# Optimization experiments

Hardware: AMD Instinct MI355X
Metric: run time of the kernel (lower is better)

## Reference

```python
import jax, jax.numpy as jnp
import numpy as np
import math

CH = 16      # scalar channels (Rs = [(16, 0)])
HEADS = 2
NB = 10      # number_of_basis for key/conv radial nets
HD = 100     # hidden width h
NBV = 3      # value radial basis (hard-coded in AttentionConvolution)
HDV = 100    # value radial hidden width
MAXR = 5.0
EPS = 1e-12  # safe-norm epsilon (r_eps analogue)


def swish(x):
    return x * jax.nn.sigmoid(x)


def cosine_basis(d, nb, max_radius):
    # CosineBasisModel basis: cos(pi/2 * (d - r_i)/step) on |.| < 1, else 0
    radii = jnp.linspace(0.0, max_radius, nb)
    step = radii[1] - radii[0]
    diff = (d[..., None] - radii) / step
    return jnp.where(jnp.abs(diff) < 1.0, jnp.cos(0.5 * math.pi * diff), 0.0)


def radial2(d, W0, W1, Wf, nb):
    # 2-hidden-layer radial MLP (L=2), swish activations, linear readout
    b = cosine_basis(d, nb, MAXR)
    hdn = swish(b @ W0)
    hdn = swish(hdn @ W1)
    return hdn @ Wf


def radial1(d, W0, Wf, nb):
    # 1-hidden-layer radial MLP (value branch, L=1)
    b = cosine_basis(d, nb, MAXR)
    return swish(b @ W0) @ Wf


def setup_inputs() -> dict:
    key = jax.random.key(0)
    ks = jax.random.split(key, 11)
    z, N = 2, 256

    def gn(k, shape, fan_in):
        return jax.random.normal(k, shape, jnp.float32) * (fan_in ** -0.5)

    return {
        "features": jax.random.normal(ks[0], (z, N, CH), jnp.float32),
        "xyz": jax.random.uniform(ks[1], (z, N, 3), jnp.float32) * MAXR,
        "Wq": gn(ks[2], (HEADS, CH, CH), CH),
        "K0": gn(ks[3], (HEADS, NB, HD), NB),
        "K1": gn(ks[4], (HEADS, HD, HD), HD),
        "Kf": gn(ks[5], (HEADS, HD, CH * CH), HD),
        "V0": gn(ks[6], (HEADS, NBV, HDV), NBV),
        "Vf": gn(ks[7], (HEADS, HDV, CH * CH), HDV),
        "C0": gn(ks[8], (NB, HD), NB),
        "C1": gn(ks[9], (HD, HD), HD),
        "Cf": gn(ks[10], (HD, CH * CH), HD),
    }


def reference(features, xyz, Wq, K0, K1, Kf, V0, Vf, C0, C1, Cf):
    z, N, ch = features.shape
    # rb - ra : rel[z, a, b] = xyz[b] - xyz[a]
    rel = xyz[:, None, :, :] - xyz[:, :, None, :]          # [z, a, b, 3]
    d = jnp.sqrt(jnp.sum(rel * rel, axis=-1) + EPS)        # [z, a, b]

    out = jnp.zeros_like(features)
    for h in range(HEADS):  # structurally distinct heads (distinct params)
        k = radial2(d, K0[h], K1[h], Kf[h], NB).reshape(z, N, N, ch, ch)
        v = radial1(d, V0[h], Vf[h], NBV).reshape(z, N, N, ch, ch)
        key_t = jnp.einsum('zabij,zbj->zabi', k, features)
        val_t = jnp.einsum('zabij,zbj->zabi', v, features)
        q = jnp.einsum('zai,oi->zao', features, Wq[h])     # Linear(Rs, Rs)
        scores = jnp.einsum('zabi,zai->zab', key_t, q) / ch
        p = jax.nn.softmax(scores, axis=-1)
        out = out + jnp.einsum('zab,zabi->zai', p, val_t)

    # final equivariant convolution: kernel(d) contracted over neighbors b
    kc = radial2(d, C0, C1, Cf, NB).reshape(z, N, N, ch, ch)
    return jnp.einsum('zabij,zbj->zai', kc, out)
```

## Files before the change

### kernel.cpp

```cpp
#include <hip/hip_runtime.h>
#include <hip/hip_fp16.h>
#include <math.h>

#define Z 2
#define NPT 256
#define CHN 16
#define NH 2
#define NBK 10
#define HD 100
#define NBV 3
#define G 512
#define VD 7.5f

__device__ __forceinline__ float swishf(float x) {
    return x / (1.0f + __expf(-x));
}

__device__ __forceinline__ float dot8(uint4 u, float4 a, float4 b) {
    float2 c0 = __half22float2(*(const __half2*)&u.x);
    float2 c1 = __half22float2(*(const __half2*)&u.y);
    float2 c2 = __half22float2(*(const __half2*)&u.z);
    float2 c3 = __half22float2(*(const __half2*)&u.w);
    return c0.x*a.x + c0.y*a.y + c1.x*a.z + c1.y*a.w
         + c2.x*b.x + c2.y*b.y + c3.x*b.z + c3.y*b.w;
}

__global__ __launch_bounds__(128)
void build_tables(const float* __restrict__ K0, const float* __restrict__ K1,
                  const float* __restrict__ C0, const float* __restrict__ C1,
                  const float* __restrict__ V0,
                  float* __restrict__ TKf, float* __restrict__ TCf,
                  float* __restrict__ TVf, float* __restrict__ out_zero) {
    int bid = blockIdx.x;
    int rep = bid >> 5;
    int g0  = (bid & 31) * 16;
    int t   = threadIdx.x;

    if (bid == 0) {
        float4* o4 = (float4*)out_zero;
        #pragma unroll
        for (int k = 0; k < 16; ++k) o4[k*128 + t] = make_float4(0.f,0.f,0.f,0.f);
    }

    if (rep >= 3) {
        const float* W0v = V0 + (rep - 3)*NBV*HD;
        float* Tf = TVf + (size_t)(rep - 3)*2*G*HD;
        if (t < HD) {
            #pragma unroll
            for (int k = 0; k < 16; ++k) {
                int gg = g0 + k;
                float d = gg * (VD / (float)(G-1));
                float s = 0.f;
                #pragma unroll
                for (int q = 0; q < NBV; ++q) {
                    float diff = (d - q*2.5f) * 0.4f;
                    float bq = (fabsf(diff) < 1.0f) ? __cosf(1.57079632679f*diff) : 0.f;
                    s += bq * W0v[q*HD + t];
                }
                float v = swishf(s);
                Tf[2*((size_t)gg*HD + t) + 0] = v;
                if (gg > 0) Tf[2*((size_t)(gg-1)*HD + t) + 1] = v;
            }
        }
        return;
    }

    const float* W0 = (rep == 0) ? K0 : (rep == 1) ? (K0 + NBK*HD) : C0;
    const float* W1 = (rep == 0) ? K1 : (rep == 1) ? (K1 + HD*HD)  : C1;
    float* Tf       = (rep == 0) ? TKf : (rep == 1) ? (TKf + 2*(size_t)G*HD) : TCf;

    __shared__ float s_b10[16][NBK];
    __shared__ __align__(16) float s_h1[HD*16];

    if (t < 16) {
        float d = (g0 + t) * (VD / (float)(G-1));
        #pragma unroll
        for (int q = 0; q < NBK; ++q) {
            float diff = (d - q*(5.0f/9.0f)) * 1.8f;
            s_b10[t][q] = (fabsf(diff) < 1.0f) ? __cosf(1.57079632679f*diff) : 0.f;
        }
    }
    __syncthreads();
    if (t < HD) {
        int n = t;
        float w[NBK];
        #pragma unroll
        for (int q = 0; q < NBK; ++q) w[q] = W0[q*HD + n];
        #pragma unroll
        for (int k = 0; k < 16; ++k) {
            float s = 0.f;
            #pragma unroll
            for (int q = 0; q < NBK; ++q) s += s_b10[k][q] * w[q];
            s_h1[n*16 + k] = swishf(s);
        }
    }
    __syncthreads();
    if (t < HD) {
        int m = t;
        float acc[16];
        #pragma unroll
        for (int k = 0; k < 16; ++k) acc[k] = 0.f;
        const float* w1 = W1 + m;
        #pragma unroll 2
        for (int n = 0; n < HD; ++n) {
            float w = w1[n*HD];
            const float4* hp = (const float4*)&s_h1[n*16];
            float4 x0 = hp[0], x1 = hp[1], x2 = hp[2], x3 = hp[3];
            acc[0]+=x0.x*w;  acc[1]+=x0.y*w;  acc[2]+=x0.z*w;  acc[3]+=x0.w*w;
            acc[4]+=x1.x*w;  acc[5]+=x1.y*w;  acc[6]+=x1.z*w;  acc[7]+=x1.w*w;
            acc[8]+=x2.x*w;  acc[9]+=x2.y*w;  acc[10]+=x2.z*w; acc[11]+=x2.w*w;
            acc[12]+=x3.x*w; acc[13]+=x3.y*w; acc[14]+=x3.z*w; acc[15]+=x3.w*w;
        }
        #pragma unroll
        for (int k = 0; k < 16; ++k) {
            float v = swishf(acc[k]);
            int gg = g0 + k;
            Tf[2*((size_t)gg*HD + m) + 0] = v;
            if (gg > 0) Tf[2*((size_t)(gg-1)*HD + m) + 1] = v;
        }
    }
}

__global__ __launch_bounds__(256)
void build_mats(const float* __restrict__ TK, const float* __restrict__ TC,
                const float* __restrict__ TV,
                const float* __restrict__ Kf, const float* __restrict__ Cf,
                const float* __restrict__ Vf,
                __half* __restrict__ MK, __half* __restrict__ MV,
                __half* __restrict__ MC) {
    int bid = blockIdx.x;
    int rep = bid >> 7;
    int g0  = (bid & 127) * 4;
    int t   = threadIdx.x;

    const float *T, *Wf;
    __half* M;
    if (rep == 0)      { T=TK;                    Wf=Kf;          M=MK; }
    else if (rep == 1) { T=TK+2*(size_t)G*HD;     Wf=Kf+HD*256;   M=MK+(size_t)G*256; }
    else if (rep == 2) { T=TC;                    Wf=Cf;          M=MC; }
    else if (rep == 3) { T=TV;                    Wf=Vf;          M=MV; }
    else               { T=TV+2*(size_t)G*HD;     Wf=Vf+HD*256;   M=MV+(size_t)G*256; }

    __shared__ float s_h[4][HD];
    for (int idx = t; idx < 4*HD; idx += 256) {
        int gp = idx / HD, m = idx - gp*HD;
        s_h[gp][m] = T[2*((size_t)(g0+gp)*HD + m)];
    }
    __syncthreads();

    float a0=0.f, a1=0.f, a2=0.f, a3=0.f;
    for (int m = 0; m < HD; ++m) {
        float w = Wf[m*256 + t];
        a0 += s_h[0][m]*w; a1 += s_h[1][m]*w;
        a2 += s_h[2][m]*w; a3 += s_h[3][m]*w;
    }
    int i = t >> 4, j = t & 15;
    int c = j >> 3, e = j & 7;
    size_t off = (size_t)(c*16 + i)*8 + e;
    M[(size_t)(g0+0)*256 + off] = __float2half(a0);
    M[(size_t)(g0+1)*256 + off] = __float2half(a1);
    M[(size_t)(g0+2)*256 + off] = __float2half(a2);
    M[(size_t)(g0+3)*256 + off] = __float2half(a3);
}

__global__ __launch_bounds__(256, 4)
void fused_attn(const float* __restrict__ f, const float* __restrict__ xyz,
                const float* __restrict__ Wq,
                const __half* __restrict__ MK, const __half* __restrict__ MV,
                float* __restrict__ attn_h) {
    int bid = blockIdx.x;
    int a  = bid & 255;
    int zh = bid >> 8;
    int h  = zh & 1;
    int z  = zh >> 1;
    int t  = threadIdx.x;

    __shared__ __align__(16) float s_f[NPT*CHN];
    __shared__ int   s_gi[NPT];
    __shared__ float s_fr[NPT];
    __shared__ float s_sc[NPT];
    __shared__ float s_q[16];
    __shared__ float s_red[8];
    __shared__ float s_red2[256];

    {
        const float4* fz = (const float4*)(f + (size_t)z*NPT*CHN);
        float4* sf = (float4*)s_f;
        for (int idx = t; idx < NPT*CHN/4; idx += 256) sf[idx] = fz[idx];
    }
    {
        float ax = xyz[(z*NPT + a)*3 + 0];
        float ay = xyz[(z*NPT + a)*3 + 1];
        float az = xyz[(z*NPT + a)*3 + 2];
        int b = t;
        float dx = xyz[(z*NPT + b)*3 + 0] - ax;
        float dy = xyz[(z*NPT + b)*3 + 1] - ay;
        float dz = xyz[(z*NPT + b)*3 + 2] - az;
        float d = sqrtf(dx*dx + dy*dy + dz*dz + 1e-12f);
        float fd = d * ((float)(G-1) / VD);
        int   gi = (int)fd;
        float fr = fd - (float)gi;
        if (gi >= G-1) { gi = G-2; fr = 1.0f; }
        s_gi[b] = gi; s_fr[b] = fr;
    }
    __syncthreads();
    if (t < CHN) {
        float s = 0.f;
        const float* wq = Wq + (h*CHN + t)*CHN;
        for (int i = 0; i < CHN; ++i) s += s_f[a*CHN + i] * wq[i];
        s_q[t] = s;
    }
    __syncthreads();

    int Gr = t >> 4;
    int i  = t & 15;
    float qi = s_q[i];
    int b0 = Gr*16;

    {
        const __half* basek = MK + (size_t)h*G*256;
        for (int k = 0; k < 16; ++k) {
            int b = b0 + k;
            const uint4* p = (const uint4*)(basek + (size_t)s_gi[b]*256) + i;
            uint4 q0 = p[0];
            uint4 q1 = p[16];
            uint4 q2 = p[32];
            uint4 q3 = p[48];
            float fr = s_fr[b];
            const float4* fp = (const float4*)&s_f[b*CHN];
            float4 f0=fp[0], f1=fp[1], f2=fp[2], f3=fp[3];
            float y0 = dot8(q0, f0, f1) + dot8(q1, f2, f3);
            float y1 = dot8(q2, f0, f1) + dot8(q3, f2, f3);
            float sc = qi * (y0 + fr*(y1 - y0));
            sc += __shfl_xor(sc, 1);
            sc += __shfl_xor(sc, 2);
            sc += __shfl_xor(sc, 4);
            sc += __shfl_xor(sc, 8);
            if (i == 0) s_sc[b] = sc * (1.0f/16.0f);
        }
    }
    __syncthreads();

    {
        float v = s_sc[t];
        float mx = v;
        for (int off = 32; off >= 1; off >>= 1) mx = fmaxf(mx, __shfl_xor(mx, off));
        int wid = t >> 6;
        if ((t & 63) == 0) s_red[wid] = mx;
        __syncthreads();
        mx = fmaxf(fmaxf(s_red[0], s_red[1]), fmaxf(s_red[2], s_red[3]));
        float e = __expf(v - mx);
        float s = e;
        for (int off = 32; off >= 1; off >>= 1) s += __shfl_xor(s, off);
        if ((t & 63) == 0) s_red[4 + wid] = s;
        __syncthreads();
        float tot = s_red[4] + s_red[5] + s_red[6] + s_red[7];
        s_sc[t] = e / tot;
    }
    __syncthreads();

    {
        const __half* basev = MV + (size_t)h*G*256;
        float o = 0.f;
        for (int k = 0; k < 16; ++k) {
            int b = b0 + k;
            const uint4* p = (const uint4*)(basev + (size_t)s_gi[b]*256) + i;
            uint4 q0 = p[0];
            uint4 q1 = p[16];
            uint4 q2 = p[32];
            uint4 q3 = p[48];
            float fr = s_fr[b];
            const float4* fp = (const float4*)&s_f[b*CHN];
            float4 f0=fp[0], f1=fp[1], f2=fp[2], f3=fp[3];
            float y0 = dot8(q0, f0, f1) + dot8(q1, f2, f3);
            float y1 = dot8(q2, f0, f1) + dot8(q3, f2, f3);
            o += s_sc[b] * (y0 + fr*(y1 - y0));
        }
        s_red2[Gr*16 + i] = o;
    }
    __syncthreads();
    if (t < 16) {
        float s = 0.f;
        for (int gp = 0; gp < 16; ++gp) s += s_red2[gp*16 + t];
        attn_h[(size_t)bid*CHN + t] = s;
    }
}

__global__ __launch_bounds__(256)
void conv_kernel(const float* __restrict__ xyz, const __half* __restrict__ MC,
                 const float* __restrict__ attn_h, float* __restrict__ out) {
    int bid = blockIdx.x;
    int bh  = bid & 1;
    int za  = bid >> 1;
    int z   = za >> 8;
    int b0g = bh * 128;
    int t   = threadIdx.x;

    __shared__ __align__(16) float s_ao[128*CHN];
    __shared__ int   s_gi[128];
    __shared__ float s_fr[128];
    __shared__ float s_red2[256];

    for (int idx = t; idx < 128*CHN; idx += 256) {
        s_ao[idx] = attn_h[(size_t)(z*NH + 0)*NPT*CHN + b0g*CHN + idx]
                  + attn_h[(size_t)(z*NH + 1)*NPT*CHN + b0g*CHN + idx];
    }
    if (t < 128) {
        int b = b0g + t;
        float dx = xyz[(z*NPT+b)*3+0] - xyz[za*3+0];
        float dy = xyz[(z*NPT+b)*3+1] - xyz[za*3+1];
        float dz = xyz[(z*NPT+b)*3+2] - xyz[za*3+2];
        float d = sqrtf(dx*dx + dy*dy + dz*dz + 1e-12f);
        float fd = d * ((float)(G-1) / VD);
        int   gi = (int)fd;
        float fr = fd - (float)gi;
        if (gi >= G-1) { gi = G-2; fr = 1.0f; }
        s_gi[t] = gi; s_fr[t] = fr;
    }
    __syncthreads();

    int Gr = t >> 4;
    int i  = t & 15;
    int l0 = Gr*8;
    {
        float o = 0.f;
        for (int k = 0; k < 8; ++k) {
            int l = l0 + k;
            const uint4* p = (const uint4*)(MC + (size_t)s_gi[l]*256) + i;
            uint4 q0 = p[0];
            uint4 q1 = p[16];
            uint4 q2 = p[32];
            uint4 q3 = p[48];
            float fr = s_fr[l];
            const float4* ap = (const float4*)&s_ao[l*CHN];
            float4 a0=ap[0], a1=ap[1], a2=ap[2], a3=ap[3];
            float y0 = dot8(q0, a0, a1) + dot8(q1, a2, a3);
            float y1 = dot8(q2, a0, a1) + dot8(q3, a2, a3);
            o += y0 + fr*(y1 - y0);
        }
        s_red2[Gr*16 + i] = o;
    }
    __syncthreads();
    if (t < 16) {
        float s = 0.f;
        for (int gp = 0; gp < 16; ++gp) s += s_red2[gp*16 + t];
        atomicAdd(out + (size_t)za*CHN + t, s);
    }
}

extern "C" void kernel_launch(void* const* d_in, const int* in_sizes, int n_in,
                              void* d_out, int out_size, void* d_ws, size_t ws_size,
                              hipStream_t stream) {
    const float* f   = (const float*)d_in[0];
    const float* xyz = (const float*)d_in[1];
    const float* Wq  = (const float*)d_in[2];
    const float* K0  = (const float*)d_in[3];
    const float* K1  = (const float*)d_in[4];
    const float* Kf  = (const float*)d_in[5];
    const float* V0  = (const float*)d_in[6];
    const float* Vf  = (const float*)d_in[7];
    const float* C0  = (const float*)d_in[8];
    const float* C1  = (const float*)d_in[9];
    const float* Cf  = (const float*)d_in[10];
    float* out = (float*)d_out;

    float2* TK2    = (float2*)d_ws;
    float2* TC2    = TK2 + (size_t)NH*G*HD;
    float2* TV2    = TC2 + (size_t)G*HD;
    __half* MK     = (__half*)(TV2 + (size_t)NH*G*HD);
    __half* MV     = MK + (size_t)NH*G*256;
    __half* MC     = MV + (size_t)NH*G*256;
    float*  attn_h = (float*)(MC + (size_t)G*256);

    build_tables<<<160,      128, 0, stream>>>(K0, K1, C0, C1, V0,
                                               (float*)TK2, (float*)TC2,
                                               (float*)TV2, out);
    build_mats  <<<640,      256, 0, stream>>>((const float*)TK2, (const float*)TC2,
                                               (const float*)TV2, Kf, Cf, Vf,
                                               MK, MV, MC);
    fused_attn  <<<Z*NH*NPT, 256, 0, stream>>>(f, xyz, Wq, MK, MV, attn_h);
    conv_kernel <<<Z*NPT*2,  256, 0, stream>>>(xyz, MC, attn_h, out);
}
```

Baseline: 132.7 us.

## Fuse radial table and matrix builds; interleave key/value matrices for single gather

Merges the two precompute kernels into one, so each block runs the radial MLP hidden layers and the final readout into half-precision matrices directly. This removes a launch and the intermediate float tables in global memory. Key and value matrices are now interleaved per grid point, so the attention kernel fetches both in one gather pass. It computes the value projections alongside the scores, keeps them in registers and reuses them after the softmax instead of gathering a second time. In exchange, the readout stage runs on 160 blocks of 128 threads instead of 640 blocks of 256, which lowers parallelism there. The extra 16 live values per thread also raise register pressure in the attention kernel.

```diff
diff --git a/kernel.cpp b/kernel.cpp
--- a/kernel.cpp
+++ b/kernel.cpp
@@ -26,11 +26,13 @@
 }
 
 __global__ __launch_bounds__(128)
-void build_tables(const float* __restrict__ K0, const float* __restrict__ K1,
-                  const float* __restrict__ C0, const float* __restrict__ C1,
-                  const float* __restrict__ V0,
-                  float* __restrict__ TKf, float* __restrict__ TCf,
-                  float* __restrict__ TVf, float* __restrict__ out_zero) {
+void build_all(const float* __restrict__ K0, const float* __restrict__ K1,
+               const float* __restrict__ Kf,
+               const float* __restrict__ C0, const float* __restrict__ C1,
+               const float* __restrict__ Cf,
+               const float* __restrict__ V0, const float* __restrict__ Vf,
+               __half* __restrict__ MKV, __half* __restrict__ MC,
+               float* __restrict__ out_zero) {
     int bid = blockIdx.x;
     int rep = bid >> 5;
     int g0  = (bid & 31) * 16;
@@ -42,9 +44,12 @@
         for (int k = 0; k < 16; ++k) o4[k*128 + t] = make_float4(0.f,0.f,0.f,0.f);
     }
 
+    __shared__ float s_b10[16][NBK];
+    __shared__ __align__(16) float s_h1[HD*16];
+    __shared__ float s_h2[16][HD];
+
     if (rep >= 3) {
         const float* W0v = V0 + (rep - 3)*NBV*HD;
-        float* Tf = TVf + (size_t)(rep - 3)*2*G*HD;
         if (t < HD) {
             #pragma unroll
             for (int k = 0; k < 16; ++k) {
@@ -57,116 +62,88 @@
                     float bq = (fabsf(diff) < 1.0f) ? __cosf(1.57079632679f*diff) : 0.f;
                     s += bq * W0v[q*HD + t];
                 }
-                float v = swishf(s);
-                Tf[2*((size_t)gg*HD + t) + 0] = v;
-                if (gg > 0) Tf[2*((size_t)(gg-1)*HD + t) + 1] = v;
+                s_h2[k][t] = swishf(s);
             }
         }
-        return;
-    }
-
-    const float* W0 = (rep == 0) ? K0 : (rep == 1) ? (K0 + NBK*HD) : C0;
-    const float* W1 = (rep == 0) ? K1 : (rep == 1) ? (K1 + HD*HD)  : C1;
-    float* Tf       = (rep == 0) ? TKf : (rep == 1) ? (TKf + 2*(size_t)G*HD) : TCf;
-
-    __shared__ float s_b10[16][NBK];
-    __shared__ __align__(16) float s_h1[HD*16];
-
-    if (t < 16) {
-        float d = (g0 + t) * (VD / (float)(G-1));
-        #pragma unroll
-        for (int q = 0; q < NBK; ++q) {
-            float diff = (d - q*(5.0f/9.0f)) * 1.8f;
-            s_b10[t][q] = (fabsf(diff) < 1.0f) ? __cosf(1.57079632679f*diff) : 0.f;
-        }
-    }
-    __syncthreads();
-    if (t < HD) {
-        int n = t;
-        float w[NBK];
-        #pragma unroll
-        for (int q = 0; q < NBK; ++q) w[q] = W0[q*HD + n];
-        #pragma unroll
-        for (int k = 0; k < 16; ++k) {
-            float s = 0.f;
-            #pragma unroll
-            for (int q = 0; q < NBK; ++q) s += s_b10[k][q] * w[q];
-            s_h1[n*16 + k] = swishf(s);
-        }
-    }
-    __syncthreads();
-    if (t < HD) {
-        int m = t;
-        float acc[16];
-        #pragma unroll
-        for (int k = 0; k < 16; ++k) acc[k] = 0.f;
-        const float* w1 = W1 + m;
-        #pragma unroll 2
-        for (int n = 0; n < HD; ++n) {
-            float w = w1[n*HD];
-            const float4* hp = (const float4*)&s_h1[n*16];
-            float4 x0 = hp[0], x1 = hp[1], x2 = hp[2], x3 = hp[3];
-            acc[0]+=x0.x*w;  acc[1]+=x0.y*w;  acc[2]+=x0.z*w;  acc[3]+=x0.w*w;
-            acc[4]+=x1.x*w;  acc[5]+=x1.y*w;  acc[6]+=x1.z*w;  acc[7]+=x1.w*w;
-            acc[8]+=x2.x*w;  acc[9]+=x2.y*w;  acc[10]+=x2.z*w; acc[11]+=x2.w*w;
-            acc[12]+=x3.x*w; acc[13]+=x3.y*w; acc[14]+=x3.z*w; acc[15]+=x3.w*w;
-        }
-        #pragma unroll
-        for (int k = 0; k < 16; ++k) {
-            float v = swishf(acc[k]);
-            int gg = g0 + k;
-            Tf[2*((size_t)gg*HD + m) + 0] = v;
-            if (gg > 0) Tf[2*((size_t)(gg-1)*HD + m) + 1] = v;
-        }
-    }
-}
-
-__global__ __launch_bounds__(256)
-void build_mats(const float* __restrict__ TK, const float* __restrict__ TC,
-                const float* __restrict__ TV,
-                const float* __restrict__ Kf, const float* __restrict__ Cf,
-                const float* __restrict__ Vf,
-                __half* __restrict__ MK, __half* __restrict__ MV,
-                __half* __restrict__ MC) {
-    int bid = blockIdx.x;
-    int rep = bid >> 7;
-    int g0  = (bid & 127) * 4;
-    int t   = threadIdx.x;
-
-    const float *T, *Wf;
-    __half* M;
-    if (rep == 0)      { T=TK;                    Wf=Kf;          M=MK; }
-    else if (rep == 1) { T=TK+2*(size_t)G*HD;     Wf=Kf+HD*256;   M=MK+(size_t)G*256; }
-    else if (rep == 2) { T=TC;                    Wf=Cf;          M=MC; }
-    else if (rep == 3) { T=TV;                    Wf=Vf;          M=MV; }
-    else               { T=TV+2*(size_t)G*HD;     Wf=Vf+HD*256;   M=MV+(size_t)G*256; }
-
-    __shared__ float s_h[4][HD];
-    for (int idx = t; idx < 4*HD; idx += 256) {
-        int gp = idx / HD, m = idx - gp*HD;
-        s_h[gp][m] = T[2*((size_t)(g0+gp)*HD + m)];
-    }
-    __syncthreads();
-
-    float a0=0.f, a1=0.f, a2=0.f, a3=0.f;
-    for (int m = 0; m < HD; ++m) {
-        float w = Wf[m*256 + t];
-        a0 += s_h[0][m]*w; a1 += s_h[1][m]*w;
-        a2 += s_h[2][m]*w; a3 += s_h[3][m]*w;
-    }
-    int i = t >> 4, j = t & 15;
-    int c = j >> 3, e = j & 7;
-    size_t off = (size_t)(c*16 + i)*8 + e;
-    M[(size_t)(g0+0)*256 + off] = __float2half(a0);
-    M[(size_t)(g0+1)*256 + off] = __float2half(a1);
-    M[(size_t)(g0+2)*256 + off] = __float2half(a2);
-    M[(size_t)(g0+3)*256 + off] = __float2half(a3);
+    } else {
+        const float* W0 = (rep == 0) ? K0 : (rep == 1) ? (K0 + NBK*HD) : C0;
+        const float* W1 = (rep == 0) ? K1 : (rep == 1) ? (K1 + HD*HD)  : C1;
+
+        if (t < 16) {
+            float d = (g0 + t) * (VD / (float)(G-1));
+            #pragma unroll
+            for (int q = 0; q < NBK; ++q) {
+                float diff = (d - q*(5.0f/9.0f)) * 1.8f;
+                s_b10[t][q] = (fabsf(diff) < 1.0f) ? __cosf(1.57079632679f*diff) : 0.f;
+            }
+        }
+        __syncthreads();
+        if (t < HD) {
+            int n = t;
+            float w[NBK];
+            #pragma unroll
+            for (int q = 0; q < NBK; ++q) w[q] = W0[q*HD + n];
+            #pragma unroll
+            for (int k = 0; k < 16; ++k) {
+                float s = 0.f;
+                #pragma unroll
+                for (int q = 0; q < NBK; ++q) s += s_b10[k][q] * w[q];
+                s_h1[n*16 + k] = swishf(s);
+            }
+        }
+        __syncthreads();
+        if (t < HD) {
+            int m = t;
+            float acc[16];
+            #pragma unroll
+            for (int k = 0; k < 16; ++k) acc[k] = 0.f;
+            const float* w1 = W1 + m;
+            #pragma unroll 2
+            for (int n = 0; n < HD; ++n) {
+                float w = w1[n*HD];
+                const float4* hp = (const float4*)&s_h1[n*16];
+                float4 x0 = hp[0], x1 = hp[1], x2 = hp[2], x3 = hp[3];
+                acc[0]+=x0.x*w;  acc[1]+=x0.y*w;  acc[2]+=x0.z*w;  acc[3]+=x0.w*w;
+                acc[4]+=x1.x*w;  acc[5]+=x1.y*w;  acc[6]+=x1.z*w;  acc[7]+=x1.w*w;
+                acc[8]+=x2.x*w;  acc[9]+=x2.y*w;  acc[10]+=x2.z*w; acc[11]+=x2.w*w;
+                acc[12]+=x3.x*w; acc[13]+=x3.y*w; acc[14]+=x3.z*w; acc[15]+=x3.w*w;
+            }
+            #pragma unroll
+            for (int k = 0; k < 16; ++k) s_h2[k][m] = swishf(acc[k]);
+        }
+    }
+    __syncthreads();
+
+    const float* Wf = (rep == 0) ? Kf
+                    : (rep == 1) ? (Kf + HD*256)
+                    : (rep == 2) ? Cf
+                    : (rep == 3) ? Vf : (Vf + HD*256);
+    __half* dst  = (rep == 2) ? MC  : (MKV + (size_t)((rep == 1 || rep == 4) ? 1 : 0)*G*512);
+    int    voff  = (rep >= 3) ? 256 : 0;
+    int    strd  = (rep == 2) ? 256 : 512;
+
+    for (int eb = 0; eb < 2; ++eb) {
+        int e = t + eb*128;
+        float facc[16];
+        #pragma unroll
+        for (int gp = 0; gp < 16; ++gp) facc[gp] = 0.f;
+        for (int m = 0; m < HD; ++m) {
+            float w = Wf[m*256 + e];
+            #pragma unroll
+            for (int gp = 0; gp < 16; ++gp) facc[gp] += s_h2[gp][m] * w;
+        }
+        int i = e >> 4, j = e & 15, c = j >> 3, eo = j & 7;
+        size_t off = (size_t)(c*16 + i)*8 + eo;
+        #pragma unroll
+        for (int gp = 0; gp < 16; ++gp)
+            dst[(size_t)(g0+gp)*strd + voff + off] = __float2half(facc[gp]);
+    }
 }
 
 __global__ __launch_bounds__(256, 4)
 void fused_attn(const float* __restrict__ f, const float* __restrict__ xyz,
                 const float* __restrict__ Wq,
-                const __half* __restrict__ MK, const __half* __restrict__ MV,
+                const __half* __restrict__ MKV,
                 float* __restrict__ attn_h) {
     int bid = blockIdx.x;
     int a  = bid & 255;
@@ -217,26 +194,32 @@
     float qi = s_q[i];
     int b0 = Gr*16;
 
-    {
-        const __half* basek = MK + (size_t)h*G*256;
+    float yv[16];
+
+    {
+        const __half* base = MKV + (size_t)h*G*512;
+        #pragma unroll
         for (int k = 0; k < 16; ++k) {
             int b = b0 + k;
-            const uint4* p = (const uint4*)(basek + (size_t)s_gi[b]*256) + i;
-            uint4 q0 = p[0];
-            uint4 q1 = p[16];
-            uint4 q2 = p[32];
-            uint4 q3 = p[48];
+            const uint4* p = (const uint4*)(base + (size_t)s_gi[b]*512) + i;
+            uint4 k0 = p[0],  k1 = p[16];
+            uint4 v0 = p[32], v1 = p[48];
+            uint4 k2 = p[64], k3 = p[80];
+            uint4 v2 = p[96], v3 = p[112];
             float fr = s_fr[b];
             const float4* fp = (const float4*)&s_f[b*CHN];
             float4 f0=fp[0], f1=fp[1], f2=fp[2], f3=fp[3];
-            float y0 = dot8(q0, f0, f1) + dot8(q1, f2, f3);
-            float y1 = dot8(q2, f0, f1) + dot8(q3, f2, f3);
-            float sc = qi * (y0 + fr*(y1 - y0));
+            float yk0 = dot8(k0, f0, f1) + dot8(k1, f2, f3);
+            float yk1 = dot8(k2, f0, f1) + dot8(k3, f2, f3);
+            float sc = qi * (yk0 + fr*(yk1 - yk0));
             sc += __shfl_xor(sc, 1);
             sc += __shfl_xor(sc, 2);
             sc += __shfl_xor(sc, 4);
             sc += __shfl_xor(sc, 8);
             if (i == 0) s_sc[b] = sc * (1.0f/16.0f);
+            float w0 = dot8(v0, f0, f1) + dot8(v1, f2, f3);
+            float w1 = dot8(v2, f0, f1) + dot8(v3, f2, f3);
+            yv[k] = w0 + fr*(w1 - w0);
         }
     }
     __syncthreads();
@@ -260,22 +243,9 @@
     __syncthreads();
 
     {
-        const __half* basev = MV + (size_t)h*G*256;
         float o = 0.f;
-        for (int k = 0; k < 16; ++k) {
-            int b = b0 + k;
-            const uint4* p = (const uint4*)(basev + (size_t)s_gi[b]*256) + i;
-            uint4 q0 = p[0];
-            uint4 q1 = p[16];
-            uint4 q2 = p[32];
-            uint4 q3 = p[48];
-            float fr = s_fr[b];
-            const float4* fp = (const float4*)&s_f[b*CHN];
-            float4 f0=fp[0], f1=fp[1], f2=fp[2], f3=fp[3];
-            float y0 = dot8(q0, f0, f1) + dot8(q1, f2, f3);
-            float y1 = dot8(q2, f0, f1) + dot8(q3, f2, f3);
-            o += s_sc[b] * (y0 + fr*(y1 - y0));
-        }
+        #pragma unroll
+        for (int k = 0; k < 16; ++k) o += s_sc[b0 + k] * yv[k];
         s_red2[Gr*16 + i] = o;
     }
     __syncthreads();
@@ -364,20 +334,12 @@
     const float* Cf  = (const float*)d_in[10];
     float* out = (float*)d_out;
 
-    float2* TK2    = (float2*)d_ws;
-    float2* TC2    = TK2 + (size_t)NH*G*HD;
-    float2* TV2    = TC2 + (size_t)G*HD;
-    __half* MK     = (__half*)(TV2 + (size_t)NH*G*HD);
-    __half* MV     = MK + (size_t)NH*G*256;
-    __half* MC     = MV + (size_t)NH*G*256;
+    __half* MKV    = (__half*)d_ws;
+    __half* MC     = MKV + (size_t)NH*G*512;
     float*  attn_h = (float*)(MC + (size_t)G*256);
 
-    build_tables<<<160,      128, 0, stream>>>(K0, K1, C0, C1, V0,
-                                               (float*)TK2, (float*)TC2,
-                                               (float*)TV2, out);
-    build_mats  <<<640,      256, 0, stream>>>((const float*)TK2, (const float*)TC2,
-                                               (const float*)TV2, Kf, Cf, Vf,
-                                               MK, MV, MC);
-    fused_attn  <<<Z*NH*NPT, 256, 0, stream>>>(f, xyz, Wq, MK, MV, attn_h);
-    conv_kernel <<<Z*NPT*2,  256, 0, stream>>>(xyz, MC, attn_h, out);
-}
+    build_all  <<<160,      128, 0, stream>>>(K0, K1, Kf, C0, C1, Cf, V0, Vf,
+                                              MKV, MC, out);
+    fused_attn <<<Z*NH*NPT, 256, 0, stream>>>(f, xyz, Wq, MKV, attn_h);
+    conv_kernel<<<Z*NPT*2,  256, 0, stream>>>(xyz, MC, attn_h, out);
+}
```

Measured after the change: 344.9 us. 160% more time.

## Interleave key and value tables and compute value projections in score pass

Applied to the files above, without the earlier changes.

Key and value matrices are now stored interleaved per grid point, so one gather fetches both. The score loop also computes the value projection per neighbor and stores it in shared memory. The second pass then reduces to a cheap weighted sum over those stored values. This removes a second round of scattered global gathers and repeated dot products, at the cost of 16 KB more shared memory per block, which may reduce occupancy under launch_bounds(256,4).

```diff
diff --git a/kernel.cpp b/kernel.cpp
--- a/kernel.cpp
+++ b/kernel.cpp
@@ -126,20 +126,22 @@
                 const float* __restrict__ TV,
                 const float* __restrict__ Kf, const float* __restrict__ Cf,
                 const float* __restrict__ Vf,
-                __half* __restrict__ MK, __half* __restrict__ MV,
-                __half* __restrict__ MC) {
+                __half* __restrict__ MKV, __half* __restrict__ MC) {
     int bid = blockIdx.x;
     int rep = bid >> 7;
     int g0  = (bid & 127) * 4;
     int t   = threadIdx.x;
 
     const float *T, *Wf;
-    __half* M;
-    if (rep == 0)      { T=TK;                    Wf=Kf;          M=MK; }
-    else if (rep == 1) { T=TK+2*(size_t)G*HD;     Wf=Kf+HD*256;   M=MK+(size_t)G*256; }
-    else if (rep == 2) { T=TC;                    Wf=Cf;          M=MC; }
-    else if (rep == 3) { T=TV;                    Wf=Vf;          M=MV; }
-    else               { T=TV+2*(size_t)G*HD;     Wf=Vf+HD*256;   M=MV+(size_t)G*256; }
+    if (rep == 0)      { T=TK;                    Wf=Kf;          }
+    else if (rep == 1) { T=TK+2*(size_t)G*HD;     Wf=Kf+HD*256;   }
+    else if (rep == 2) { T=TC;                    Wf=Cf;          }
+    else if (rep == 3) { T=TV;                    Wf=Vf;          }
+    else               { T=TV+2*(size_t)G*HD;     Wf=Vf+HD*256;   }
+    __half* dst = (rep == 2) ? MC
+                : (MKV + (size_t)((rep == 1 || rep == 4) ? 1 : 0)*G*512);
+    int voff = (rep >= 3) ? 256 : 0;
+    int strd = (rep == 2) ? 256 : 512;
 
     __shared__ float s_h[4][HD];
     for (int idx = t; idx < 4*HD; idx += 256) {
@@ -154,19 +156,18 @@
         a0 += s_h[0][m]*w; a1 += s_h[1][m]*w;
         a2 += s_h[2][m]*w; a3 += s_h[3][m]*w;
     }
-    int i = t >> 4, j = t & 15;
-    int c = j >> 3, e = j & 7;
-    size_t off = (size_t)(c*16 + i)*8 + e;
-    M[(size_t)(g0+0)*256 + off] = __float2half(a0);
-    M[(size_t)(g0+1)*256 + off] = __float2half(a1);
-    M[(size_t)(g0+2)*256 + off] = __float2half(a2);
-    M[(size_t)(g0+3)*256 + off] = __float2half(a3);
+    int i = t >> 4, j = t & 15, c = j >> 3, eo = j & 7;
+    size_t off = (size_t)(c*16 + i)*8 + eo;
+    dst[(size_t)(g0+0)*strd + voff + off] = __float2half(a0);
+    dst[(size_t)(g0+1)*strd + voff + off] = __float2half(a1);
+    dst[(size_t)(g0+2)*strd + voff + off] = __float2half(a2);
+    dst[(size_t)(g0+3)*strd + voff + off] = __float2half(a3);
 }
 
 __global__ __launch_bounds__(256, 4)
 void fused_attn(const float* __restrict__ f, const float* __restrict__ xyz,
                 const float* __restrict__ Wq,
-                const __half* __restrict__ MK, const __half* __restrict__ MV,
+                const __half* __restrict__ MKV,
                 float* __restrict__ attn_h) {
     int bid = blockIdx.x;
     int a  = bid & 255;
@@ -176,6 +177,7 @@
     int t  = threadIdx.x;
 
     __shared__ __align__(16) float s_f[NPT*CHN];
+    __shared__ float s_yv[NPT*16];
     __shared__ int   s_gi[NPT];
     __shared__ float s_fr[NPT];
     __shared__ float s_sc[NPT];
@@ -218,25 +220,29 @@
     int b0 = Gr*16;
 
     {
-        const __half* basek = MK + (size_t)h*G*256;
+        const __half* base = MKV + (size_t)h*G*512;
+        #pragma unroll 2
         for (int k = 0; k < 16; ++k) {
             int b = b0 + k;
-            const uint4* p = (const uint4*)(basek + (size_t)s_gi[b]*256) + i;
-            uint4 q0 = p[0];
-            uint4 q1 = p[16];
-            uint4 q2 = p[32];
-            uint4 q3 = p[48];
+            const uint4* p = (const uint4*)(base + (size_t)s_gi[b]*512) + i;
+            uint4 k0 = p[0],  k1 = p[16];
+            uint4 v0 = p[32], v1 = p[48];
+            uint4 k2 = p[64], k3 = p[80];
+            uint4 v2 = p[96], v3 = p[112];
             float fr = s_fr[b];
             const float4* fp = (const float4*)&s_f[b*CHN];
             float4 f0=fp[0], f1=fp[1], f2=fp[2], f3=fp[3];
-            float y0 = dot8(q0, f0, f1) + dot8(q1, f2, f3);
-            float y1 = dot8(q2, f0, f1) + dot8(q3, f2, f3);
-            float sc = qi * (y0 + fr*(y1 - y0));
+            float yk0 = dot8(k0, f0, f1) + dot8(k1, f2, f3);
+            float yk1 = dot8(k2, f0, f1) + dot8(k3, f2, f3);
+            float sc = qi * (yk0 + fr*(yk1 - yk0));
             sc += __shfl_xor(sc, 1);
             sc += __shfl_xor(sc, 2);
             sc += __shfl_xor(sc, 4);
             sc += __shfl_xor(sc, 8);
             if (i == 0) s_sc[b] = sc * (1.0f/16.0f);
+            float w0 = dot8(v0, f0, f1) + dot8(v1, f2, f3);
+            float w1 = dot8(v2, f0, f1) + dot8(v3, f2, f3);
+            s_yv[b*16 + i] = w0 + fr*(w1 - w0);
         }
     }
     __syncthreads();
@@ -260,22 +266,9 @@
     __syncthreads();
 
     {
-        const __half* basev = MV + (size_t)h*G*256;
         float o = 0.f;
-        for (int k = 0; k < 16; ++k) {
-            int b = b0 + k;
-            const uint4* p = (const uint4*)(basev + (size_t)s_gi[b]*256) + i;
-            uint4 q0 = p[0];
-            uint4 q1 = p[16];
-            uint4 q2 = p[32];
-            uint4 q3 = p[48];
-            float fr = s_fr[b];
-            const float4* fp = (const float4*)&s_f[b*CHN];
-            float4 f0=fp[0], f1=fp[1], f2=fp[2], f3=fp[3];
-            float y0 = dot8(q0, f0, f1) + dot8(q1, f2, f3);
-            float y1 = dot8(q2, f0, f1) + dot8(q3, f2, f3);
-            o += s_sc[b] * (y0 + fr*(y1 - y0));
-        }
+        #pragma unroll
+        for (int k = 0; k < 16; ++k) o += s_sc[b0 + k] * s_yv[(b0 + k)*16 + i];
         s_red2[Gr*16 + i] = o;
     }
     __syncthreads();
@@ -367,9 +360,8 @@
     float2* TK2    = (float2*)d_ws;
     float2* TC2    = TK2 + (size_t)NH*G*HD;
     float2* TV2    = TC2 + (size_t)G*HD;
-    __half* MK     = (__half*)(TV2 + (size_t)NH*G*HD);
-    __half* MV     = MK + (size_t)NH*G*256;
-    __half* MC     = MV + (size_t)NH*G*256;
+    __half* MKV    = (__half*)(TV2 + (size_t)NH*G*HD);
+    __half* MC     = MKV + (size_t)NH*G*512;
     float*  attn_h = (float*)(MC + (size_t)G*256);
 
     build_tables<<<160,      128, 0, stream>>>(K0, K1, C0, C1, V0,
@@ -377,7 +369,7 @@
                                                (float*)TV2, out);
     build_mats  <<<640,      256, 0, stream>>>((const float*)TK2, (const float*)TC2,
                                                (const float*)TV2, Kf, Cf, Vf,
-                                               MK, MV, MC);
-    fused_attn  <<<Z*NH*NPT, 256, 0, stream>>>(f, xyz, Wq, MK, MV, attn_h);
+                                               MKV, MC);
+    fused_attn  <<<Z*NH*NPT, 256, 0, stream>>>(f, xyz, Wq, MKV, attn_h);
     conv_kernel <<<Z*NPT*2,  256, 0, stream>>>(xyz, MC, attn_h, out);
 }
```

Measured after the change: 132.5 us. No clear change (-0.2%).
